# Performance work log

Hardware: AMD Instinct MI355X
Metric: run time of the kernel (lower is better)

## Reference

```python
import jax, jax.numpy as jnp
import numpy as np

N = 100000   # nodes
E = 3200000  # edges (avg degree 32)
G = 512      # graphs in batch
F_IN = 10
H = 30


def setup_inputs() -> dict:
    key = jax.random.key(0)
    ks = jax.random.split(key, 14)
    x = jax.random.normal(ks[0], (N, F_IN), dtype=jnp.float32)
    edge_index = jax.random.randint(ks[1], (2, E), 0, N, dtype=jnp.int64)
    batch = jnp.sort(jax.random.randint(ks[2], (N,), 0, G, dtype=jnp.int64))
    edge_weights = jnp.ones((E,), dtype=jnp.float32)
    s = 0.1
    W1 = jax.random.normal(ks[3], (F_IN, H), jnp.float32) * s
    b1 = jnp.zeros((H,), jnp.float32)
    W2 = jax.random.normal(ks[4], (H, H), jnp.float32) * s
    b2 = jnp.zeros((H,), jnp.float32)
    W3 = jax.random.normal(ks[5], (H, H), jnp.float32) * s
    b3 = jnp.zeros((H,), jnp.float32)
    LW1 = jax.random.normal(ks[6], (H, 10), jnp.float32) * s
    Lb1 = jnp.zeros((10,), jnp.float32)
    LW2 = jax.random.normal(ks[7], (10, 2), jnp.float32) * s
    Lb2 = jnp.zeros((2,), jnp.float32)
    return dict(x=x, edge_index=edge_index, batch=batch, edge_weights=edge_weights,
                W1=W1, b1=b1, W2=W2, b2=b2, W3=W3, b3=b3,
                LW1=LW1, Lb1=Lb1, LW2=LW2, Lb2=Lb2)


def reference(x, edge_index, batch, edge_weights, W1, b1, W2, b2, W3, b3, LW1, Lb1, LW2, Lb2):
    n = x.shape[0]
    row, col = edge_index[0], edge_index[1]
    # PyG gcn_norm: add self-loops with weight 1, symmetric normalization
    loop = jnp.arange(n)
    row_f = jnp.concatenate([row, loop])
    col_f = jnp.concatenate([col, loop])
    w_f = jnp.concatenate([edge_weights, jnp.ones((n,), edge_weights.dtype)])
    deg = jax.ops.segment_sum(w_f, col_f, num_segments=n)
    dis = jnp.where(deg > 0, jax.lax.rsqrt(jnp.where(deg > 0, deg, 1.0)), 0.0)
    norm = dis[row_f] * w_f * dis[col_f]  # [E+N]

    def gcn(h, W, b):
        h = h @ W  # [N, out]
        agg = jax.ops.segment_sum(norm[:, None] * h[row_f], col_f, num_segments=n)
        return agg + b

    h = jax.nn.relu(gcn(x, W1, b1))
    h = jax.nn.relu(gcn(h, W2, b2))
    h = jax.nn.relu(gcn(h, W3, b3))  # embedding [N, 30]
    pooled = jax.ops.segment_max(h, batch, num_segments=G)  # [G, 30]
    out = jax.nn.relu(pooled @ LW1 + Lb1) @ LW2 + Lb2  # [G, 2]
    return out
```

## Files before the change

kernel.cpp:

```cpp
#include <hip/hip_runtime.h>
#include <hip/hip_bf16.h>


#define WG 256
#define CAP 9216
#define T_EDGES 16384

__global__ void k_init(int* bcur, float* pooled, int nb16, int pooledN) {
    int i = blockIdx.x * blockDim.x + threadIdx.x;
    if (i < nb16) bcur[i] = 0;
    if (i < pooledN) pooled[i] = 0.0f;
}

__global__ __launch_bounds__(1024)
void k_bucket(const int* __restrict__ row, const int* __restrict__ col,
              const float* __restrict__ w,
              int* bcur, int2* __restrict__ buck, int E, int NB) {
    __shared__ int hist[512];
    __shared__ int base[512];
    int tid = threadIdx.x;
    for (int i = tid; i < NB; i += 1024) hist[i] = 0;
    __syncthreads();
    int start = blockIdx.x * T_EDGES;
    int end = min(start + T_EDGES, E);
    for (int i = start + tid; i < end; i += 1024)
        atomicAdd(&hist[col[i] >> 8], 1);
    __syncthreads();
    for (int i = tid; i < NB; i += 1024) {
        int h = hist[i];
        base[i] = (h > 0) ? atomicAdd(&bcur[i * 16], h) : 0;
        hist[i] = 0;
    }
    __syncthreads();
    for (int i = start + tid; i < end; i += 1024) {
        int c = col[i];
        int b = c >> 8;
        int off = atomicAdd(&hist[b], 1);
        int pos = base[b] + off;
        if (pos < CAP) {
            int2 pk;
            pk.x = (c & 255) | (row[i] << 8);
            pk.y = __float_as_int(w[i]);
            buck[(size_t)b * CAP + pos] = pk;
        }
    }
}

__global__ __launch_bounds__(1024)
void k_fuse(const int* __restrict__ bcur, const int2* __restrict__ buck,
            float* __restrict__ dis, int* __restrict__ ptr,
            int2* __restrict__ csr, int N, int NB) {
    __shared__ int lc[256];
    __shared__ float lw[256];
    __shared__ int sh[256];
    __shared__ int cur[256];
    __shared__ int sb[512];
    int b = blockIdx.x;
    int tid = threadIdx.x;
    if (tid < 512) sb[tid] = (tid < NB) ? min(bcur[tid * 16], CAP) : 0;
    if (tid < 256) { lc[tid] = 0; lw[tid] = 0.0f; }
    __syncthreads();
    for (int off = 1; off < 512; off <<= 1) {
        int v = (tid < 512 && tid >= off) ? sb[tid - off] : 0;
        __syncthreads();
        if (tid < 512) sb[tid] += v;
        __syncthreads();
    }
    int m = min(bcur[b * 16], CAP);
    int bbase = sb[b] - m;
    if (b == 0 && tid == 0) ptr[N] = sb[511];
    const int2* bp = buck + (size_t)b * CAP;
    for (int i = tid; i < m; i += 1024) {
        int2 pk = bp[i];
        int lcol = pk.x & 255;
        atomicAdd(&lc[lcol], 1);
        atomicAdd(&lw[lcol], __int_as_float(pk.y));
    }
    __syncthreads();
    int lcnt = 0;
    if (tid < 256) { lcnt = lc[tid]; sh[tid] = lcnt; }
    __syncthreads();
    for (int off = 1; off < 256; off <<= 1) {
        int t = (tid >= off && tid < 256) ? sh[tid - off] : 0;
        __syncthreads();
        if (tid < 256) sh[tid] += t;
        __syncthreads();
    }
    int node = (b << 8) + tid;
    if (tid < 256) {
        int base = bbase + sh[tid] - lcnt;
        cur[tid] = base;
        if (node < N) {
            ptr[node] = base;
            float d = 1.0f + lw[tid];
            dis[node] = (d > 0.0f) ? (1.0f / sqrtf(d)) : 0.0f;
        }
    }
    __syncthreads();
    for (int i = tid; i < m; i += 1024) {
        int2 pk = bp[i];
        int lcol = pk.x & 255;
        int pos = atomicAdd(&cur[lcol], 1);
        int2 rec;
        rec.x = (int)(((unsigned)pk.x) >> 8);
        rec.y = pk.y;
        csr[pos] = rec;
    }
}

__global__ void k_stage(const float* __restrict__ x, const float* __restrict__ dis,
                        float* __restrict__ xp, int n) {
    int gid = blockIdx.x * blockDim.x + threadIdx.x;
    int node = gid >> 4, f = gid & 15;
    if (node < n)
        xp[(size_t)node * 16 + f] = (f < 10) ? dis[node] * x[(size_t)node * 10 + f] : 0.0f;
}

__global__ void k_agg16(const float* __restrict__ xp, const float* __restrict__ dis,
                        const int* __restrict__ ptr, const int2* __restrict__ csr,
                        float* __restrict__ y, int n) {
    int wid = (blockIdx.x * blockDim.x + threadIdx.x) >> 6;
    int lane = threadIdx.x & 63;
    int f = lane & 15;
    int laneq = lane & 48;
    int node = 4 * wid + (lane >> 4);
    bool valid = node < n;
    int s = 0, e = 0;
    if (valid) { s = ptr[node]; e = ptr[node + 1]; }
    int len = e - s;
    int m01 = max(__shfl(len, 0, 64), __shfl(len, 16, 64));
    int m23 = max(__shfl(len, 32, 64), __shfl(len, 48, 64));
    int maxlen = max(m01, m23);
    float a0 = 0.0f, a1 = 0.0f, a2 = 0.0f, a3 = 0.0f;
    for (int off = 0; off < maxlen; off += 16) {
        int idxv = 0; float nrmv = 0.0f;
        if (off + f < len) {
            int2 v = csr[s + off + f];
            idxv = v.x;
            nrmv = __int_as_float(v.y);
        }
#pragma unroll
        for (int j = 0; j < 16; j += 4) {
            int r0 = __shfl(idxv, laneq | j, 64);       float w0 = __shfl(nrmv, laneq | j, 64);
            int r1 = __shfl(idxv, laneq | (j + 1), 64); float w1 = __shfl(nrmv, laneq | (j + 1), 64);
            int r2 = __shfl(idxv, laneq | (j + 2), 64); float w2 = __shfl(nrmv, laneq | (j + 2), 64);
            int r3 = __shfl(idxv, laneq | (j + 3), 64); float w3 = __shfl(nrmv, laneq | (j + 3), 64);
            a0 = fmaf(w0, xp[(size_t)r0 * 16 + f], a0);
            a1 = fmaf(w1, xp[(size_t)r1 * 16 + f], a1);
            a2 = fmaf(w2, xp[(size_t)r2 * 16 + f], a2);
            a3 = fmaf(w3, xp[(size_t)r3 * 16 + f], a3);
        }
    }
    if (valid) {
        float acc = (a0 + a1) + (a2 + a3);
        float r = dis[node] * (acc + xp[(size_t)node * 16 + f]);
        y[(size_t)node * 16 + f] = r;
    }
}

__global__ __launch_bounds__(256)
void k_lin1(const float* __restrict__ y, const float* __restrict__ W1,
            const float* __restrict__ b1, const float* __restrict__ W2,
            const float* __restrict__ dis, float* __restrict__ out, int n) {
    __shared__ float W1s[10 * 32];
    __shared__ float W2s[30 * 32];
    __shared__ float b1s[32];
    __shared__ float ys[8][16];
    __shared__ float hs[8][32];
    int tid = threadIdx.x;
    for (int i = tid; i < 10 * 32; i += 256) { int k = i >> 5, f = i & 31; W1s[i] = (f < 30) ? W1[k * 30 + f] : 0.0f; }
    for (int i = tid; i < 30 * 32; i += 256) { int k = i >> 5, f = i & 31; W2s[i] = (f < 30) ? W2[k * 30 + f] : 0.0f; }
    if (tid < 32) b1s[tid] = (tid < 30) ? b1[tid] : 0.0f;
    int n8 = tid >> 5, f = tid & 31;
    int node = blockIdx.x * 8 + n8;
    __syncthreads();
    if (node < n && f < 16) ys[n8][f] = y[(size_t)node * 16 + f];
    __syncthreads();
    if (node < n) {
        float h = b1s[f];
#pragma unroll
        for (int k = 0; k < 10; k++) h += ys[n8][k] * W1s[k * 32 + f];
        h = fmaxf(h, 0.0f);
        if (f >= 30) h = 0.0f;
        hs[n8][f] = h;
    }
    __syncthreads();
    if (node < n) {
        float o = 0.0f;
#pragma unroll
        for (int k = 0; k < 30; k++) o += hs[n8][k] * W2s[k * 32 + f];
        out[(size_t)node * 32 + f] = o * dis[node];
    }
}

__global__ void k_matmul30(const float* __restrict__ in,
                           const float* __restrict__ W, const float* __restrict__ dis,
                           float* __restrict__ out, int n) {
    __shared__ float Ws[30 * 30];
    for (int idx = threadIdx.x; idx < 30 * 30; idx += blockDim.x) Ws[idx] = W[idx];
    __syncthreads();
    int gid = blockIdx.x * blockDim.x + threadIdx.x;
    int node = gid >> 5;
    int f = gid & 31;
    if (node < n) {
        float acc = 0.0f;
        if (f < 30) {
            const float* ip = in + (size_t)node * 32;
#pragma unroll
            for (int k = 0; k < 30; k++) acc += ip[k] * Ws[k * 30 + f];
            acc *= dis[node];
        }
        out[(size_t)node * 32 + f] = acc;
    }
}

__global__ void k_agg(const float* __restrict__ hw, const float* __restrict__ dis,
                      const int* __restrict__ ptr, const int2* __restrict__ csr,
                      const float* __restrict__ bias,
                      float* __restrict__ out, int n) {
    int wid = (blockIdx.x * blockDim.x + threadIdx.x) >> 6;
    int lane = threadIdx.x & 63;
    int f = lane & 31;
    int lane32 = lane & 32;
    int node = 2 * wid + (lane >> 5);
    bool valid = node < n;
    int s = 0, e = 0;
    if (valid) { s = ptr[node]; e = ptr[node + 1]; }
    int len = e - s;
    int maxlen = max(__shfl(len, 0, 64), __shfl(len, 32, 64));
    float a0 = 0.0f, a1 = 0.0f, a2 = 0.0f, a3 = 0.0f;
    for (int off = 0; off < maxlen; off += 32) {
        int idxv = 0; float nrmv = 0.0f;
        if (off + f < len) {
            int2 v = csr[s + off + f];
            idxv = v.x;
            nrmv = __int_as_float(v.y);
        }
#pragma unroll
        for (int j = 0; j < 32; j += 4) {
            int r0 = __shfl(idxv, lane32 | j, 64);       float w0 = __shfl(nrmv, lane32 | j, 64);
            int r1 = __shfl(idxv, lane32 | (j + 1), 64); float w1 = __shfl(nrmv, lane32 | (j + 1), 64);
            int r2 = __shfl(idxv, lane32 | (j + 2), 64); float w2 = __shfl(nrmv, lane32 | (j + 2), 64);
            int r3 = __shfl(idxv, lane32 | (j + 3), 64); float w3 = __shfl(nrmv, lane32 | (j + 3), 64);
            a0 = fmaf(w0, hw[(size_t)r0 * 32 + f], a0);
            a1 = fmaf(w1, hw[(size_t)r1 * 32 + f], a1);
            a2 = fmaf(w2, hw[(size_t)r2 * 32 + f], a2);
            a3 = fmaf(w3, hw[(size_t)r3 * 32 + f], a3);
        }
    }
    if (valid && f < 30) {
        float acc = (a0 + a1) + (a2 + a3);
        float r = dis[node] * (acc + hw[(size_t)node * 32 + f]);
        out[(size_t)node * 32 + f] = fmaxf(r + bias[f], 0.0f);
    }
}

__global__ void k_pool(const float* __restrict__ h, const int* __restrict__ batch,
                       float* pooled, int n) {
    int gid = blockIdx.x * blockDim.x + threadIdx.x;
    int chunk = gid >> 5;
    int f = gid & 31;
    int n0 = chunk * 64;
    if (n0 >= n || f >= 30) return;
    int end = min(n0 + 64, n);
    int curg = batch[n0];
    float m = 0.0f;
    for (int i = n0; i < end; i++) {
        int g = batch[i];
        if (g != curg) {
            atomicMax((int*)&pooled[curg * 32 + f], __float_as_int(m));
            m = 0.0f;
            curg = g;
        }
        m = fmaxf(m, h[(size_t)i * 32 + f]);
    }
    atomicMax((int*)&pooled[curg * 32 + f], __float_as_int(m));
}

__global__ void k_mlp(const float* __restrict__ pooled,
                      const float* __restrict__ LW1, const float* __restrict__ Lb1,
                      const float* __restrict__ LW2, const float* __restrict__ Lb2,
                      float* __restrict__ out, int G) {
    int g = blockIdx.x * blockDim.x + threadIdx.x;
    if (g >= G) return;
    float p[30];
#pragma unroll
    for (int k = 0; k < 30; k++) p[k] = pooled[g * 32 + k];
    float o0 = Lb2[0], o1 = Lb2[1];
#pragma unroll
    for (int j = 0; j < 10; j++) {
        float hj = Lb1[j];
#pragma unroll
        for (int k = 0; k < 30; k++) hj += p[k] * LW1[k * 10 + j];
        hj = fmaxf(hj, 0.0f);
        o0 += hj * LW2[j * 2 + 0];
        o1 += hj * LW2[j * 2 + 1];
    }
    out[g * 2 + 0] = o0;
    out[g * 2 + 1] = o1;
}

extern "C" void kernel_launch(void* const* d_in, const int* in_sizes, int n_in,
                              void* d_out, int out_size, void* d_ws, size_t ws_size,
                              hipStream_t stream) {
    const float* x     = (const float*)d_in[0];
    const int*   ei    = (const int*)d_in[1];
    const int*   batch = (const int*)d_in[2];
    const float* ew    = (const float*)d_in[3];
    const float* W1 = (const float*)d_in[4];  const float* b1  = (const float*)d_in[5];
    const float* W2 = (const float*)d_in[6];  const float* b2  = (const float*)d_in[7];
    const float* W3 = (const float*)d_in[8];  const float* b3  = (const float*)d_in[9];
    const float* LW1 = (const float*)d_in[10]; const float* Lb1 = (const float*)d_in[11];
    const float* LW2 = (const float*)d_in[12]; const float* Lb2 = (const float*)d_in[13];
    float* out = (float*)d_out;

    const int N = in_sizes[2];
    const int E = in_sizes[3];
    const int G = out_size / 2;
    const int* row = ei;
    const int* col = ei + E;

    const int NB = (N + 255) >> 8;

    char* p = (char*)d_ws;
    auto carve = [&](size_t bytes) -> void* {
        void* r = (void*)p;
        p += (bytes + 255) & ~(size_t)255;
        return r;
    };
    int*   ptr       = (int*)carve((size_t)(N + 1) * 4);
    float* dis       = (float*)carve((size_t)N * 4);
    int*   bcur      = (int*)carve((size_t)NB * 16 * 4);
    int2*  csr       = (int2*)carve((size_t)E * 8);
    size_t buckBytes = (size_t)NB * CAP * 8;
    size_t featBytes = (size_t)N * 32 * 4 * 2;
    char*  regionA   = (char*)carve(buckBytes > featBytes ? buckBytes : featBytes);
    int2*  buck      = (int2*)regionA;
    float* bufA      = (float*)regionA;
    float* xp        = (float*)regionA;
    float* y16       = (float*)(regionA + (size_t)N * 16 * 4);
    float* bufB      = (float*)(regionA + (size_t)N * 32 * 4);
    float* pooled    = (float*)carve((size_t)G * 32 * 4);

    int initN = (NB * 16 > G * 32) ? NB * 16 : G * 32;

    k_init<<<(initN + WG - 1) / WG, WG, 0, stream>>>(bcur, pooled, NB * 16, G * 32);
    k_bucket<<<(E + T_EDGES - 1) / T_EDGES, 1024, 0, stream>>>(row, col, ew, bcur, buck, E, NB);
    k_fuse<<<NB, 1024, 0, stream>>>(bcur, buck, dis, ptr, csr, N, NB);

    int agg_grid   = (int)(((size_t)((N + 1) / 2) * 64 + WG - 1) / WG);
    int agg16_grid = (int)(((size_t)((N + 3) / 4) * 64 + WG - 1) / WG);
    int mm_grid    = (int)(((size_t)N * 32 + WG - 1) / WG);

    k_stage<<<(int)(((size_t)N * 16 + WG - 1) / WG), WG, 0, stream>>>(x, dis, xp, N);
    k_agg16<<<agg16_grid, WG, 0, stream>>>(xp, dis, ptr, csr, y16, N);
    k_lin1<<<(N + 7) / 8, 256, 0, stream>>>(y16, W1, b1, W2, dis, bufB, N);
    k_agg<<<agg_grid, WG, 0, stream>>>(bufB, dis, ptr, csr, b2, bufA, N);
    k_matmul30<<<mm_grid, WG, 0, stream>>>(bufA, W3, dis, bufB, N);
    k_agg<<<agg_grid, WG, 0, stream>>>(bufB, dis, ptr, csr, b3, bufA, N);

    int pool_grid = (int)((((size_t)(N + 63) / 64) * 32 + WG - 1) / WG);
    k_pool<<<pool_grid, WG, 0, stream>>>(bufA, batch, pooled, N);
    k_mlp<<<(G + WG - 1) / WG, WG, 0, stream>>>(pooled, LW1, Lb1, LW2, Lb2, out, G);
}
```

Measured before the change: 424.4 us.

## Assign one wavefront per node in 30-wide aggregation and batch gather loads

The 30-feature aggregation kernel now uses a full 64-lane wavefront per destination node instead of two nodes per wavefront. The two halves split the node's edges, with even and odd edges going to each half, and their partial sums are combined with a cross-half shuffle. Both aggregation kernels now issue all 16 gathers per chunk into register arrays before the FMAs, to raise memory-level parallelism, and they get launch bounds. This doubles the number of waves and puts half-idle lanes on the csr loads, and the larger register footprint may limit occupancy.

```diff
diff --git a/kernel.cpp b/kernel.cpp
--- a/kernel.cpp
+++ b/kernel.cpp
@@ -116,9 +116,10 @@
         xp[(size_t)node * 16 + f] = (f < 10) ? dis[node] * x[(size_t)node * 10 + f] : 0.0f;
 }
 
-__global__ void k_agg16(const float* __restrict__ xp, const float* __restrict__ dis,
-                        const int* __restrict__ ptr, const int2* __restrict__ csr,
-                        float* __restrict__ y, int n) {
+__global__ __launch_bounds__(256, 4)
+void k_agg16(const float* __restrict__ xp, const float* __restrict__ dis,
+             const int* __restrict__ ptr, const int2* __restrict__ csr,
+             float* __restrict__ y, int n) {
     int wid = (blockIdx.x * blockDim.x + threadIdx.x) >> 6;
     int lane = threadIdx.x & 63;
     int f = lane & 15;
@@ -139,16 +140,19 @@
             idxv = v.x;
             nrmv = __int_as_float(v.y);
         }
+        float wt[16], vt[16];
+#pragma unroll
+        for (int j = 0; j < 16; j++) {
+            int r = __shfl(idxv, laneq | j, 64);
+            wt[j] = __shfl(nrmv, laneq | j, 64);
+            vt[j] = xp[(size_t)r * 16 + f];
+        }
 #pragma unroll
         for (int j = 0; j < 16; j += 4) {
-            int r0 = __shfl(idxv, laneq | j, 64);       float w0 = __shfl(nrmv, laneq | j, 64);
-            int r1 = __shfl(idxv, laneq | (j + 1), 64); float w1 = __shfl(nrmv, laneq | (j + 1), 64);
-            int r2 = __shfl(idxv, laneq | (j + 2), 64); float w2 = __shfl(nrmv, laneq | (j + 2), 64);
-            int r3 = __shfl(idxv, laneq | (j + 3), 64); float w3 = __shfl(nrmv, laneq | (j + 3), 64);
-            a0 = fmaf(w0, xp[(size_t)r0 * 16 + f], a0);
-            a1 = fmaf(w1, xp[(size_t)r1 * 16 + f], a1);
-            a2 = fmaf(w2, xp[(size_t)r2 * 16 + f], a2);
-            a3 = fmaf(w3, xp[(size_t)r3 * 16 + f], a3);
+            a0 = fmaf(wt[j],     vt[j],     a0);
+            a1 = fmaf(wt[j + 1], vt[j + 1], a1);
+            a2 = fmaf(wt[j + 2], vt[j + 2], a2);
+            a3 = fmaf(wt[j + 3], vt[j + 3], a3);
         }
     }
     if (valid) {
@@ -214,44 +218,50 @@
     }
 }
 
-__global__ void k_agg(const float* __restrict__ hw, const float* __restrict__ dis,
-                      const int* __restrict__ ptr, const int2* __restrict__ csr,
-                      const float* __restrict__ bias,
-                      float* __restrict__ out, int n) {
+__global__ __launch_bounds__(256, 4)
+void k_agg(const float* __restrict__ hw, const float* __restrict__ dis,
+           const int* __restrict__ ptr, const int2* __restrict__ csr,
+           const float* __restrict__ bias,
+           float* __restrict__ out, int n) {
     int wid = (blockIdx.x * blockDim.x + threadIdx.x) >> 6;
     int lane = threadIdx.x & 63;
+    if (wid >= n) return;
     int f = lane & 31;
-    int lane32 = lane & 32;
-    int node = 2 * wid + (lane >> 5);
-    bool valid = node < n;
-    int s = 0, e = 0;
-    if (valid) { s = ptr[node]; e = ptr[node + 1]; }
-    int len = e - s;
-    int maxlen = max(__shfl(len, 0, 64), __shfl(len, 32, 64));
+    int half = lane >> 5;
+    int s = ptr[wid];
+    int e = ptr[wid + 1];
     float a0 = 0.0f, a1 = 0.0f, a2 = 0.0f, a3 = 0.0f;
-    for (int off = 0; off < maxlen; off += 32) {
+    for (int base = s; base < e; base += 32) {
         int idxv = 0; float nrmv = 0.0f;
-        if (off + f < len) {
-            int2 v = csr[s + off + f];
+        int src = base + lane;
+        if (lane < 32 && src < e) {
+            int2 v = csr[src];
             idxv = v.x;
             nrmv = __int_as_float(v.y);
         }
-#pragma unroll
-        for (int j = 0; j < 32; j += 4) {
-            int r0 = __shfl(idxv, lane32 | j, 64);       float w0 = __shfl(nrmv, lane32 | j, 64);
-            int r1 = __shfl(idxv, lane32 | (j + 1), 64); float w1 = __shfl(nrmv, lane32 | (j + 1), 64);
-            int r2 = __shfl(idxv, lane32 | (j + 2), 64); float w2 = __shfl(nrmv, lane32 | (j + 2), 64);
-            int r3 = __shfl(idxv, lane32 | (j + 3), 64); float w3 = __shfl(nrmv, lane32 | (j + 3), 64);
-            a0 = fmaf(w0, hw[(size_t)r0 * 32 + f], a0);
-            a1 = fmaf(w1, hw[(size_t)r1 * 32 + f], a1);
-            a2 = fmaf(w2, hw[(size_t)r2 * 32 + f], a2);
-            a3 = fmaf(w3, hw[(size_t)r3 * 32 + f], a3);
-        }
-    }
-    if (valid && f < 30) {
-        float acc = (a0 + a1) + (a2 + a3);
-        float r = dis[node] * (acc + hw[(size_t)node * 32 + f]);
-        out[(size_t)node * 32 + f] = fmaxf(r + bias[f], 0.0f);
+        float wt[16], vt[16];
+#pragma unroll
+        for (int j = 0; j < 16; j++) {
+            int sl = 2 * j + half;
+            int r = __shfl(idxv, sl, 64);
+            wt[j] = __shfl(nrmv, sl, 64);
+            vt[j] = hw[(size_t)r * 32 + f];
+        }
+#pragma unroll
+        for (int j = 0; j < 16; j += 4) {
+            a0 = fmaf(wt[j],     vt[j],     a0);
+            a1 = fmaf(wt[j + 1], vt[j + 1], a1);
+            a2 = fmaf(wt[j + 2], vt[j + 2], a2);
+            a3 = fmaf(wt[j + 3], vt[j + 3], a3);
+        }
+    }
+    float acc = (a0 + a1) + (a2 + a3);
+    acc += __shfl_xor(acc, 32, 64);
+    float dc = dis[wid];
+    float r = dc * (acc + hw[(size_t)wid * 32 + f]);
+    if (half == 0 && f < 30) {
+        r += bias[f];
+        out[(size_t)wid * 32 + f] = fmaxf(r, 0.0f);
     }
 }
 
@@ -348,7 +358,7 @@
     k_bucket<<<(E + T_EDGES - 1) / T_EDGES, 1024, 0, stream>>>(row, col, ew, bcur, buck, E, NB);
     k_fuse<<<NB, 1024, 0, stream>>>(bcur, buck, dis, ptr, csr, N, NB);
 
-    int agg_grid   = (int)(((size_t)((N + 1) / 2) * 64 + WG - 1) / WG);
+    int agg_grid   = (int)(((size_t)N * 64 + WG - 1) / WG);
     int agg16_grid = (int)(((size_t)((N + 3) / 4) * 64 + WG - 1) / WG);
     int mm_grid    = (int)(((size_t)N * 32 + WG - 1) / WG);
 
```

Measured after the change: 410.7 us. 1.03x faster.
